# Kernel tuning notes

Measured on AMD Instinct MI355X. Metric: run time of the kernel, lower is better.

The kernel has to match this reference:

```python
import jax, jax.numpy as jnp
import numpy as np

N_NODES = 6144
IN_FEATURES = 256
N_HEADS = 4
N_HIDDEN = 64  # out_features, concat=False
LEAKY_SLOPE = 0.2
NEG_INF = -9e16


def setup_inputs() -> dict:
    key = jax.random.key(0)
    k1, k2, k3, k4 = jax.random.split(key, 4)
    h = jax.random.normal(k1, (N_NODES, IN_FEATURES), dtype=jnp.float32)
    adj_mat = jax.random.randint(k2, (N_NODES, N_NODES), 0, 2, dtype=jnp.int32)
    W = jax.random.normal(k3, (IN_FEATURES, N_HEADS * N_HIDDEN), dtype=jnp.float32) * 0.06
    a = jax.random.normal(k4, (N_HEADS, 2 * N_HIDDEN, 1), dtype=jnp.float32) * 0.1
    return {"h": h, "adj_mat": adj_mat, "W": W, "a": a}


def reference(h, adj_mat, W, a):
    n_nodes = h.shape[0]
    # linear transform, dropout is identity in eval mode
    ht = (h @ W).reshape(n_nodes, N_HEADS, N_HIDDEN).transpose(1, 0, 2)  # [H, N, d]
    a_src = a[:, :N_HIDDEN, 0]   # [H, d]
    a_tgt = a[:, N_HIDDEN:, 0]   # [H, d]
    src = jnp.einsum('hnd,hd->hn', ht, a_src)  # [H, N]
    tgt = jnp.einsum('hnd,hd->hn', ht, a_tgt)  # [H, N]
    e = src[:, :, None] + tgt[:, None, :]       # [H, N, N]
    e = jnp.where(e >= 0, e, LEAKY_SLOPE * e)    # leaky relu
    e = jnp.where(adj_mat[None, :, :] > 0, e, jnp.float32(NEG_INF))
    attention = jax.nn.softmax(e, axis=-1)       # [H, N, N]
    h_prime = jnp.einsum('hij,hjd->hid', attention, ht)  # [H, N, d]
    return h_prime.mean(axis=0)                  # [N, d] (concat=False)
```

## Files before the change

### kernel.cpp

```cpp
#include <hip/hip_runtime.h>
#include <hip/hip_bf16.h>

#define N_NODES 6144
#define IN_F 256
#define N_HEADS 4
#define N_HID 64
#define NWORDS32 (N_NODES / 32)

typedef __attribute__((ext_vector_type(8))) short short8;
typedef __attribute__((ext_vector_type(4))) float floatx4;

__device__ __forceinline__ short f2bf_bits(float f) {
    union { float f; unsigned u; } v; v.f = f;
    unsigned r = v.u + 0x7fffu + ((v.u >> 16) & 1u);
    return (short)(r >> 16);
}

__global__ __launch_bounds__(256) void pack_adj_kernel(
    const int* __restrict__ adj, unsigned long long* __restrict__ mask64, int nwords)
{
    const int gtid = blockIdx.x * 256 + threadIdx.x;
    const int wave = gtid >> 6;
    const int lane = threadIdx.x & 63;
    const int nwaves = (gridDim.x * 256) >> 6;
    for (int w = wave; w < nwords; w += nwaves) {
        const int v = adj[(size_t)w * 64 + lane];
        const unsigned long long b = __ballot(v > 0);
        if (lane == 0) mask64[w] = b;
    }
}

__global__ __launch_bounds__(256) void ht_gemm_kernel(
    const float* __restrict__ h, const float* __restrict__ W,
    const float* __restrict__ a, short* __restrict__ htF,
    float* __restrict__ srcv, float* __restrict__ tgtv)
{
    __shared__ float As[32][68];
    __shared__ float Bs[32][68];
    __shared__ float redS[64][16];
    __shared__ float redT[64][16];

    const int head = blockIdx.y;
    const int i0 = blockIdx.x * 64;
    const int tid = threadIdx.x;
    const int tx = tid & 15, ty = tid >> 4;

    float acc[4][4] = {};

    for (int k0 = 0; k0 < IN_F; k0 += 32) {
        __syncthreads();
        #pragma unroll
        for (int it = 0; it < 2; ++it) {
            int l = it * 256 + tid;
            int m = l >> 3;
            int kq = l & 7;
            const float4 v = *(const float4*)(h + (i0 + m) * IN_F + k0 + kq * 4);
            As[kq*4+0][m] = v.x; As[kq*4+1][m] = v.y;
            As[kq*4+2][m] = v.z; As[kq*4+3][m] = v.w;
        }
        #pragma unroll
        for (int it = 0; it < 2; ++it) {
            int l = it * 256 + tid;
            int k = l >> 4;
            int nq = l & 15;
            *(float4*)&Bs[k][nq*4] = *(const float4*)(W + (k0 + k) * 256 + head * 64 + nq * 4);
        }
        __syncthreads();
        #pragma unroll
        for (int kk = 0; kk < 32; ++kk) {
            const float4 av = *(const float4*)&As[kk][ty*4];
            const float4 bv = *(const float4*)&Bs[kk][tx*4];
            const float aa[4] = {av.x, av.y, av.z, av.w};
            const float bb[4] = {bv.x, bv.y, bv.z, bv.w};
            #pragma unroll
            for (int r = 0; r < 4; ++r)
                #pragma unroll
                for (int c = 0; c < 4; ++c)
                    acc[r][c] = fmaf(aa[r], bb[c], acc[r][c]);
        }
    }

    #pragma unroll
    for (int r = 0; r < 4; ++r)
        #pragma unroll
        for (int c2 = 0; c2 < 4; ++c2) {
            const int d = tx * 4 + c2;
            const int j = i0 + ty * 4 + r;
            const int jt = j >> 5, q = (j >> 3) & 3, u = j & 7;
            const int c = d >> 4, n = d & 15;
            const size_t F = (((((size_t)head * 192 + jt) * 4 + c) * 16 + n) * 4 + q) * 8 + u;
            htF[F] = f2bf_bits(acc[r][c2]);
        }

    float as_[4], at_[4];
    #pragma unroll
    for (int c = 0; c < 4; ++c) {
        as_[c] = a[head * 128 + tx * 4 + c];
        at_[c] = a[head * 128 + 64 + tx * 4 + c];
    }
    #pragma unroll
    for (int r = 0; r < 4; ++r) {
        float ps = 0.f, pt = 0.f;
        #pragma unroll
        for (int c = 0; c < 4; ++c) {
            ps = fmaf(acc[r][c], as_[c], ps);
            pt = fmaf(acc[r][c], at_[c], pt);
        }
        redS[ty*4+r][tx] = ps;
        redT[ty*4+r][tx] = pt;
    }
    __syncthreads();
    if (tid < 128) {
        const int row = tid & 63;
        const float* src = (tid < 64) ? &redS[row][0] : &redT[row][0];
        float s = 0.f;
        #pragma unroll
        for (int x = 0; x < 16; ++x) s += src[x];
        if (tid < 64) srcv[head * N_NODES + i0 + row] = s;
        else          tgtv[head * N_NODES + i0 + row] = s;
    }
}

__global__ __launch_bounds__(256) void gat_main_kernel(
    const unsigned* __restrict__ mask32, const short* __restrict__ htF,
    const float* __restrict__ srcv, const float* __restrict__ tgtv,
    float* __restrict__ pnum, float* __restrict__ pden, int jlen)
{
    __shared__ unsigned smask[16][197];

    const int lane = threadIdx.x;
    const int head = threadIdx.y;
    const int jc = blockIdx.y;
    const int i0 = blockIdx.x * 16;
    const int m = lane & 15, quad = lane >> 4;
    const int row = i0 + m;
    const int jbase = jc * jlen;
    const int nw = jlen >> 5;

    const int tid = head * 64 + lane;
    for (int t = tid; t < 16 * nw; t += 256) {
        const int r = t / nw, w = t - r * nw;
        smask[r][w] = mask32[(size_t)(i0 + r) * NWORDS32 + (jbase >> 5) + w];
    }
    __syncthreads();

    const float src_val = srcv[head * N_NODES + row];
    const float* tgt_row = tgtv + head * N_NODES;
    const short* fb = htF + ((size_t)(head * 192 + (jbase >> 5)) * 4) * 512 + (m * 4 + quad) * 8;

    floatx4 acc0 = {0,0,0,0}, acc1 = {0,0,0,0}, acc2 = {0,0,0,0}, acc3 = {0,0,0,0};
    float denp = 0.f;

    for (int w = 0; w < nw; ++w) {
        const int jb = jbase + w * 32 + quad * 8;
        const unsigned bits = (smask[m][w] >> (quad * 8)) & 0xffu;
        const float4 t0 = *(const float4*)(tgt_row + jb);
        const float4 t1 = *(const float4*)(tgt_row + jb + 4);
        const short8 b0 = *(const short8*)(fb + (size_t)w * 2048);
        const short8 b1 = *(const short8*)(fb + (size_t)w * 2048 + 512);
        const short8 b2 = *(const short8*)(fb + (size_t)w * 2048 + 1024);
        const short8 b3 = *(const short8*)(fb + (size_t)w * 2048 + 1536);
        const float tv[8] = {t0.x, t0.y, t0.z, t0.w, t1.x, t1.y, t1.z, t1.w};

        short8 af;
        #pragma unroll
        for (int u = 0; u < 8; ++u) {
            float e = src_val + tv[u];
            e = fmaxf(e, 0.2f * e);
            float ww = __expf(e);
            ww = (bits & (1u << u)) ? ww : 0.f;
            denp += ww;
            af[u] = f2bf_bits(ww);
        }

        acc0 = __builtin_amdgcn_mfma_f32_16x16x32_bf16(af, b0, acc0, 0, 0, 0);
        acc1 = __builtin_amdgcn_mfma_f32_16x16x32_bf16(af, b1, acc1, 0, 0, 0);
        acc2 = __builtin_amdgcn_mfma_f32_16x16x32_bf16(af, b2, acc2, 0, 0, 0);
        acc3 = __builtin_amdgcn_mfma_f32_16x16x32_bf16(af, b3, acc3, 0, 0, 0);
    }

    const int slot = jc * N_HEADS + head;

    denp += __shfl_xor(denp, 16, 64);
    denp += __shfl_xor(denp, 32, 64);
    if (quad == 0) pden[slot * N_NODES + row] = denp;

    #pragma unroll
    for (int r = 0; r < 4; ++r) {
        const int gi = i0 + quad * 4 + r;
        float* np_ = pnum + ((size_t)slot * N_NODES + gi) * N_HID + (lane & 15);
        np_[0]  = acc0[r];
        np_[16] = acc1[r];
        np_[32] = acc2[r];
        np_[48] = acc3[r];
    }
}

__global__ __launch_bounds__(256) void finalize_kernel(
    const float* __restrict__ pnum, const float* __restrict__ pden,
    float* __restrict__ out, int js)
{
    const int idx = blockIdx.x * 256 + threadIdx.x;
    if (idx >= N_NODES * N_HID) return;
    const int i = idx >> 6;
    const int d = idx & 63;
    float s = 0.f;
    for (int hh = 0; hh < N_HEADS; ++hh) {
        float ns = 0.f, ds = 0.f;
        for (int jc = 0; jc < js; ++jc) {
            const int slot = jc * N_HEADS + hh;
            ns += pnum[((size_t)slot * N_NODES + i) * N_HID + d];
            ds += pden[slot * N_NODES + i];
        }
        s += ns / ds;
    }
    out[idx] = 0.25f * s;
}

extern "C" void kernel_launch(void* const* d_in, const int* in_sizes, int n_in,
                              void* d_out, int out_size, void* d_ws, size_t ws_size,
                              hipStream_t stream)
{
    const float* h   = (const float*)d_in[0];
    const int*   adj = (const int*)d_in[1];
    const float* W   = (const float*)d_in[2];
    const float* a   = (const float*)d_in[3];
    float* out = (float*)d_out;

    char* ws = (char*)d_ws;
    short* htF = (short*)ws;
    size_t off = (size_t)N_HEADS * N_HID * N_NODES * 2;
    float* srcv = (float*)(ws + off);  off += (size_t)N_HEADS * N_NODES * 4;
    float* tgtv = (float*)(ws + off);  off += (size_t)N_HEADS * N_NODES * 4;
    const int nwords64 = N_NODES * N_NODES / 64;
    unsigned long long* mask64 = (unsigned long long*)(ws + off);
    off += (size_t)nwords64 * 8;

    const size_t per_js = (size_t)N_HEADS * N_NODES * N_HID * 4 + (size_t)N_HEADS * N_NODES * 4;
    int js = 4;
    while (js > 1 && off + (size_t)js * per_js > ws_size) js >>= 1;
    const int jlen = N_NODES / js;

    float* pnum = (float*)(ws + off);  off += (size_t)js * N_HEADS * N_NODES * N_HID * 4;
    float* pden = (float*)(ws + off);

    pack_adj_kernel<<<2048, 256, 0, stream>>>(adj, mask64, nwords64);
    ht_gemm_kernel<<<dim3(N_NODES / 64, N_HEADS), 256, 0, stream>>>(h, W, a, htF, srcv, tgtv);
    gat_main_kernel<<<dim3(N_NODES / 16, js), dim3(64, 4), 0, stream>>>(
        (const unsigned*)mask64, htF, srcv, tgtv, pnum, pden, jlen);
    finalize_kernel<<<dim3((N_NODES * N_HID) / 256), 256, 0, stream>>>(pnum, pden, out, js);
}
```

Measured before the change: 335.0 us.

## Factor exp of leaky-relu into precomputed exps, switch to fp16 MFMA

The per-edge exp is replaced by products of precomputed exponentials: exp(s)*exp(t) when s+t>=0, otherwise exp(0.2s)*exp(0.2t). This removes transcendental work from the inner loop at the cost of two target tables. The denominator moves into an extra MFMA against a ones vector, and operands change from bf16 to fp16 with packed conversion. Other changes: the j-split defaults to 8 with a floor of 2, the projection GEMM uses smaller tiles, and the mask packer is unrolled. Without max subtraction, the exp products can overflow or underflow fp16 and fp32 for large logits, and the js floor of 2 can exceed workspace.

```diff
diff --git a/kernel.cpp b/kernel.cpp
--- a/kernel.cpp
+++ b/kernel.cpp
@@ -9,51 +9,50 @@
 
 typedef __attribute__((ext_vector_type(8))) short short8;
 typedef __attribute__((ext_vector_type(4))) float floatx4;
-
-__device__ __forceinline__ short f2bf_bits(float f) {
-    union { float f; unsigned u; } v; v.f = f;
-    unsigned r = v.u + 0x7fffu + ((v.u >> 16) & 1u);
-    return (short)(r >> 16);
-}
+typedef _Float16 half2_t __attribute__((ext_vector_type(2)));
+typedef _Float16 half8_t __attribute__((ext_vector_type(8)));
 
 __global__ __launch_bounds__(256) void pack_adj_kernel(
     const int* __restrict__ adj, unsigned long long* __restrict__ mask64, int nwords)
 {
-    const int gtid = blockIdx.x * 256 + threadIdx.x;
-    const int wave = gtid >> 6;
+    const int wave = (blockIdx.x * 256 + threadIdx.x) >> 6;
     const int lane = threadIdx.x & 63;
     const int nwaves = (gridDim.x * 256) >> 6;
-    for (int w = wave; w < nwords; w += nwaves) {
-        const int v = adj[(size_t)w * 64 + lane];
-        const unsigned long long b = __ballot(v > 0);
-        if (lane == 0) mask64[w] = b;
+    for (int w = wave * 8; w + 7 < nwords; w += nwaves * 8) {
+        int v[8];
+        #pragma unroll
+        for (int k = 0; k < 8; ++k) v[k] = adj[(size_t)(w + k) * 64 + lane];
+        unsigned long long b[8];
+        #pragma unroll
+        for (int k = 0; k < 8; ++k) b[k] = __ballot(v[k] > 0);
+        if (lane == 0) {
+            #pragma unroll
+            for (int k = 0; k < 8; ++k) mask64[w + k] = b[k];
+        }
     }
 }
 
 __global__ __launch_bounds__(256) void ht_gemm_kernel(
     const float* __restrict__ h, const float* __restrict__ W,
     const float* __restrict__ a, short* __restrict__ htF,
-    float* __restrict__ srcv, float* __restrict__ tgtv)
-{
-    __shared__ float As[32][68];
+    float* __restrict__ srcv, float* __restrict__ tgtE1, float* __restrict__ tgtE2)
+{
+    __shared__ float As[32][34];
     __shared__ float Bs[32][68];
-    __shared__ float redS[64][16];
-    __shared__ float redT[64][16];
+    __shared__ float redS[32][16];
+    __shared__ float redT[32][16];
 
     const int head = blockIdx.y;
-    const int i0 = blockIdx.x * 64;
+    const int i0 = blockIdx.x * 32;
     const int tid = threadIdx.x;
     const int tx = tid & 15, ty = tid >> 4;
 
-    float acc[4][4] = {};
+    float acc[2][4] = {};
 
     for (int k0 = 0; k0 < IN_F; k0 += 32) {
         __syncthreads();
-        #pragma unroll
-        for (int it = 0; it < 2; ++it) {
-            int l = it * 256 + tid;
-            int m = l >> 3;
-            int kq = l & 7;
+        {
+            const int m = tid >> 3, kq = tid & 7;
             const float4 v = *(const float4*)(h + (i0 + m) * IN_F + k0 + kq * 4);
             As[kq*4+0][m] = v.x; As[kq*4+1][m] = v.y;
             As[kq*4+2][m] = v.z; As[kq*4+3][m] = v.w;
@@ -61,19 +60,18 @@
         #pragma unroll
         for (int it = 0; it < 2; ++it) {
             int l = it * 256 + tid;
-            int k = l >> 4;
-            int nq = l & 15;
+            int k = l >> 4, nq = l & 15;
             *(float4*)&Bs[k][nq*4] = *(const float4*)(W + (k0 + k) * 256 + head * 64 + nq * 4);
         }
         __syncthreads();
         #pragma unroll
         for (int kk = 0; kk < 32; ++kk) {
-            const float4 av = *(const float4*)&As[kk][ty*4];
+            const float2 av = *(const float2*)&As[kk][ty*2];
             const float4 bv = *(const float4*)&Bs[kk][tx*4];
-            const float aa[4] = {av.x, av.y, av.z, av.w};
+            const float aa[2] = {av.x, av.y};
             const float bb[4] = {bv.x, bv.y, bv.z, bv.w};
             #pragma unroll
-            for (int r = 0; r < 4; ++r)
+            for (int r = 0; r < 2; ++r)
                 #pragma unroll
                 for (int c = 0; c < 4; ++c)
                     acc[r][c] = fmaf(aa[r], bb[c], acc[r][c]);
@@ -81,15 +79,16 @@
     }
 
     #pragma unroll
-    for (int r = 0; r < 4; ++r)
+    for (int r = 0; r < 2; ++r)
         #pragma unroll
         for (int c2 = 0; c2 < 4; ++c2) {
             const int d = tx * 4 + c2;
-            const int j = i0 + ty * 4 + r;
+            const int j = i0 + ty * 2 + r;
             const int jt = j >> 5, q = (j >> 3) & 3, u = j & 7;
             const int c = d >> 4, n = d & 15;
             const size_t F = (((((size_t)head * 192 + jt) * 4 + c) * 16 + n) * 4 + q) * 8 + u;
-            htF[F] = f2bf_bits(acc[r][c2]);
+            const _Float16 hv = (_Float16)acc[r][c2];
+            htF[F] = *(const short*)&hv;
         }
 
     float as_[4], at_[4];
@@ -99,34 +98,39 @@
         at_[c] = a[head * 128 + 64 + tx * 4 + c];
     }
     #pragma unroll
-    for (int r = 0; r < 4; ++r) {
+    for (int r = 0; r < 2; ++r) {
         float ps = 0.f, pt = 0.f;
         #pragma unroll
         for (int c = 0; c < 4; ++c) {
             ps = fmaf(acc[r][c], as_[c], ps);
             pt = fmaf(acc[r][c], at_[c], pt);
         }
-        redS[ty*4+r][tx] = ps;
-        redT[ty*4+r][tx] = pt;
+        redS[ty*2+r][tx] = ps;
+        redT[ty*2+r][tx] = pt;
     }
     __syncthreads();
-    if (tid < 128) {
-        const int row = tid & 63;
-        const float* src = (tid < 64) ? &redS[row][0] : &redT[row][0];
+    if (tid < 64) {
+        const int row = tid & 31;
+        const float* src = (tid < 32) ? &redS[row][0] : &redT[row][0];
         float s = 0.f;
         #pragma unroll
         for (int x = 0; x < 16; ++x) s += src[x];
-        if (tid < 64) srcv[head * N_NODES + i0 + row] = s;
-        else          tgtv[head * N_NODES + i0 + row] = s;
+        if (tid < 32) {
+            srcv[head * N_NODES + i0 + row] = s;
+        } else {
+            tgtE1[head * N_NODES + i0 + row] = __expf(s);
+            tgtE2[head * N_NODES + i0 + row] = __expf(0.2f * s);
+        }
     }
 }
 
 __global__ __launch_bounds__(256) void gat_main_kernel(
     const unsigned* __restrict__ mask32, const short* __restrict__ htF,
-    const float* __restrict__ srcv, const float* __restrict__ tgtv,
+    const float* __restrict__ srcv, const float* __restrict__ tgtE1,
+    const float* __restrict__ tgtE2,
     float* __restrict__ pnum, float* __restrict__ pden, int jlen)
 {
-    __shared__ unsigned smask[16][197];
+    __shared__ unsigned smask[16][97];
 
     const int lane = threadIdx.x;
     const int head = threadIdx.y;
@@ -144,51 +148,69 @@
     }
     __syncthreads();
 
-    const float src_val = srcv[head * N_NODES + row];
-    const float* tgt_row = tgtv + head * N_NODES;
+    const float sv = srcv[head * N_NODES + row];
+    const float e1s = __expf(sv);
+    const float e2s = __expf(0.2f * sv);
+    const float* tE1 = tgtE1 + head * N_NODES;
+    const float* tE2 = tgtE2 + head * N_NODES;
     const short* fb = htF + ((size_t)(head * 192 + (jbase >> 5)) * 4) * 512 + (m * 4 + quad) * 8;
 
+    half8_t bones;
+    #pragma unroll
+    for (int u = 0; u < 8; ++u) bones[u] = (_Float16)1.0f;
+
     floatx4 acc0 = {0,0,0,0}, acc1 = {0,0,0,0}, acc2 = {0,0,0,0}, acc3 = {0,0,0,0};
-    float denp = 0.f;
+    floatx4 accD = {0,0,0,0};
 
     for (int w = 0; w < nw; ++w) {
         const int jb = jbase + w * 32 + quad * 8;
         const unsigned bits = (smask[m][w] >> (quad * 8)) & 0xffu;
-        const float4 t0 = *(const float4*)(tgt_row + jb);
-        const float4 t1 = *(const float4*)(tgt_row + jb + 4);
-        const short8 b0 = *(const short8*)(fb + (size_t)w * 2048);
-        const short8 b1 = *(const short8*)(fb + (size_t)w * 2048 + 512);
-        const short8 b2 = *(const short8*)(fb + (size_t)w * 2048 + 1024);
-        const short8 b3 = *(const short8*)(fb + (size_t)w * 2048 + 1536);
-        const float tv[8] = {t0.x, t0.y, t0.z, t0.w, t1.x, t1.y, t1.z, t1.w};
-
-        short8 af;
+        const float4 p1a = *(const float4*)(tE1 + jb);
+        const float4 p1b = *(const float4*)(tE1 + jb + 4);
+        const float4 p2a = *(const float4*)(tE2 + jb);
+        const float4 p2b = *(const float4*)(tE2 + jb + 4);
+        const half8_t b0 = *(const half8_t*)(fb + (size_t)w * 2048);
+        const half8_t b1 = *(const half8_t*)(fb + (size_t)w * 2048 + 512);
+        const half8_t b2 = *(const half8_t*)(fb + (size_t)w * 2048 + 1024);
+        const half8_t b3 = *(const half8_t*)(fb + (size_t)w * 2048 + 1536);
+
+        const float E1[8] = {p1a.x, p1a.y, p1a.z, p1a.w, p1b.x, p1b.y, p1b.z, p1b.w};
+        const float E2[8] = {p2a.x, p2a.y, p2a.z, p2a.w, p2b.x, p2b.y, p2b.z, p2b.w};
+
+        float wv[8];
         #pragma unroll
         for (int u = 0; u < 8; ++u) {
-            float e = src_val + tv[u];
-            e = fmaxf(e, 0.2f * e);
-            float ww = __expf(e);
-            ww = (bits & (1u << u)) ? ww : 0.f;
-            denp += ww;
-            af[u] = f2bf_bits(ww);
-        }
-
-        acc0 = __builtin_amdgcn_mfma_f32_16x16x32_bf16(af, b0, acc0, 0, 0, 0);
-        acc1 = __builtin_amdgcn_mfma_f32_16x16x32_bf16(af, b1, acc1, 0, 0, 0);
-        acc2 = __builtin_amdgcn_mfma_f32_16x16x32_bf16(af, b2, acc2, 0, 0, 0);
-        acc3 = __builtin_amdgcn_mfma_f32_16x16x32_bf16(af, b3, acc3, 0, 0, 0);
+            const float p1 = e1s * E1[u];
+            float ww = (p1 >= 1.0f) ? p1 : e2s * E2[u];
+            wv[u] = (bits & (1u << u)) ? ww : 0.f;
+        }
+        half8_t af;
+        #pragma unroll
+        for (int u = 0; u < 4; ++u) {
+            const half2_t p = __builtin_bit_cast(half2_t,
+                __builtin_amdgcn_cvt_pkrtz(wv[2*u], wv[2*u+1]));
+            af[2*u] = p[0]; af[2*u+1] = p[1];
+        }
+
+        acc0 = __builtin_amdgcn_mfma_f32_16x16x32_f16(af, b0, acc0, 0, 0, 0);
+        acc1 = __builtin_amdgcn_mfma_f32_16x16x32_f16(af, b1, acc1, 0, 0, 0);
+        acc2 = __builtin_amdgcn_mfma_f32_16x16x32_f16(af, b2, acc2, 0, 0, 0);
+        acc3 = __builtin_amdgcn_mfma_f32_16x16x32_f16(af, b3, acc3, 0, 0, 0);
+        accD = __builtin_amdgcn_mfma_f32_16x16x32_f16(af, bones, accD, 0, 0, 0);
     }
 
     const int slot = jc * N_HEADS + head;
 
-    denp += __shfl_xor(denp, 16, 64);
-    denp += __shfl_xor(denp, 32, 64);
-    if (quad == 0) pden[slot * N_NODES + row] = denp;
+    if (m == 0) {
+        #pragma unroll
+        for (int r = 0; r < 4; ++r)
+            pden[slot * N_NODES + i0 + quad * 4 + r] = accD[r];
+    }
 
     #pragma unroll
     for (int r = 0; r < 4; ++r) {
         const int gi = i0 + quad * 4 + r;
-        float* np_ = pnum + ((size_t)slot * N_NODES + gi) * N_HID + (lane & 15);
+        float* np_ = pnum + ((size_t)slot * N_NODES + gi) * N_HID + m;
         np_[0]  = acc0[r];
         np_[16] = acc1[r];
         np_[32] = acc2[r];
@@ -230,23 +252,24 @@
     char* ws = (char*)d_ws;
     short* htF = (short*)ws;
     size_t off = (size_t)N_HEADS * N_HID * N_NODES * 2;
-    float* srcv = (float*)(ws + off);  off += (size_t)N_HEADS * N_NODES * 4;
-    float* tgtv = (float*)(ws + off);  off += (size_t)N_HEADS * N_NODES * 4;
+    float* srcv  = (float*)(ws + off);  off += (size_t)N_HEADS * N_NODES * 4;
+    float* tgtE1 = (float*)(ws + off);  off += (size_t)N_HEADS * N_NODES * 4;
+    float* tgtE2 = (float*)(ws + off);  off += (size_t)N_HEADS * N_NODES * 4;
     const int nwords64 = N_NODES * N_NODES / 64;
     unsigned long long* mask64 = (unsigned long long*)(ws + off);
     off += (size_t)nwords64 * 8;
 
     const size_t per_js = (size_t)N_HEADS * N_NODES * N_HID * 4 + (size_t)N_HEADS * N_NODES * 4;
-    int js = 4;
-    while (js > 1 && off + (size_t)js * per_js > ws_size) js >>= 1;
+    int js = 8;
+    while (js > 2 && off + (size_t)js * per_js > ws_size) js >>= 1;
     const int jlen = N_NODES / js;
 
     float* pnum = (float*)(ws + off);  off += (size_t)js * N_HEADS * N_NODES * N_HID * 4;
     float* pden = (float*)(ws + off);
 
     pack_adj_kernel<<<2048, 256, 0, stream>>>(adj, mask64, nwords64);
-    ht_gemm_kernel<<<dim3(N_NODES / 64, N_HEADS), 256, 0, stream>>>(h, W, a, htF, srcv, tgtv);
+    ht_gemm_kernel<<<dim3(N_NODES / 32, N_HEADS), 256, 0, stream>>>(h, W, a, htF, srcv, tgtE1, tgtE2);
     gat_main_kernel<<<dim3(N_NODES / 16, js), dim3(64, 4), 0, stream>>>(
-        (const unsigned*)mask64, htF, srcv, tgtv, pnum, pden, jlen);
+        (const unsigned*)mask64, htF, srcv, tgtE1, tgtE2, pnum, pden, jlen);
     finalize_kernel<<<dim3((N_NODES * N_HID) / 256), 256, 0, stream>>>(pnum, pden, out, js);
 }
```

Measured after the change: 353.8 us. 5.6% more time.
